# Optimization experiments

Measured on AMD Instinct MI355X. Metric: run time of the kernel, lower is better.

Reference implementation:

```python
import jax, jax.numpy as jnp
import numpy as np

EPS = 1e-5

def group_norm(x, w, b, groups):
    B, C, H, W = x.shape
    xg = x.reshape(B, groups, -1)
    mu = xg.mean(-1, keepdims=True)
    var = xg.var(-1, keepdims=True)
    xn = ((xg - mu) * jax.lax.rsqrt(var + EPS)).reshape(B, C, H, W)
    return xn * w[None, :, None, None] + b[None, :, None, None]

def gelu(x):
    return jax.nn.gelu(x, approximate=False)

def setup_inputs() -> dict:
    key = jax.random.key(0)
    ks = iter(jax.random.split(key, 64))
    B, H, W = 16, 64, 64
    dims = [128, 256, 512]
    hid = [32, 64, 128]  # max(d//4,16)
    total = 896
    sq = 112  # 896 // 8
    inp = {}
    inp["d0"] = jax.random.normal(next(ks), (B, dims[0], H, W), jnp.float32)
    inp["d1"] = jax.random.normal(next(ks), (B, dims[1], H, W), jnp.float32)
    inp["d2"] = jax.random.normal(next(ks), (B, dims[2], H, W), jnp.float32)
    for i, d in enumerate(dims):
        inp[f"gn{i}_w"] = jnp.ones((d,), jnp.float32)
        inp[f"gn{i}_b"] = jnp.zeros((d,), jnp.float32)
        inp[f"g{i}_w1"] = jax.random.normal(next(ks), (hid[i], d), jnp.float32) * 0.02
        inp[f"g{i}_b1"] = jnp.zeros((hid[i],), jnp.float32)
        inp[f"g{i}_w2"] = jax.random.normal(next(ks), (d, hid[i]), jnp.float32) * 0.02
        inp[f"g{i}_b2"] = jnp.zeros((d,), jnp.float32)
    inp["cn_w"] = jnp.ones((total,), jnp.float32)
    inp["cn_b"] = jnp.zeros((total,), jnp.float32)
    for name in ("ge", "le"):
        inp[f"{name}_w1"] = jax.random.normal(next(ks), (sq, total), jnp.float32) * 0.02
        inp[f"{name}_b1"] = jnp.zeros((sq,), jnp.float32)
        inp[f"{name}_w2"] = jax.random.normal(next(ks), (total, sq), jnp.float32) * 0.02
        inp[f"{name}_b2"] = jnp.zeros((total,), jnp.float32)
    inp["r_w"] = jax.random.normal(next(ks), (2, total), jnp.float32) * 0.02
    inp["r_b"] = jnp.zeros((2,), jnp.float32)
    inp["temp"] = jnp.ones((1,), jnp.float32)
    inp["gamma"] = jnp.ones((1,), jnp.float32) * 0.1
    return inp

def reference(d0, d1, d2,
              gn0_w, gn0_b, gn1_w, gn1_b, gn2_w, gn2_b,
              g0_w1, g0_b1, g0_w2, g0_b2,
              g1_w1, g1_b1, g1_w2, g1_b2,
              g2_w1, g2_b1, g2_w2, g2_b2,
              cn_w, cn_b,
              ge_w1, ge_b1, ge_w2, ge_b2,
              le_w1, le_b1, le_w2, le_b2,
              r_w, r_b, temp, gamma):
    def gate(d, w1, b1, w2, b2):
        p = d.mean((2, 3))                       # (B, C) avg pool
        g = jax.nn.sigmoid(gelu(p @ w1.T + b1) @ w2.T + b2)
        return d * g[:, :, None, None]

    d0 = group_norm(d0, gn0_w, gn0_b, 32)
    d1 = group_norm(d1, gn1_w, gn1_b, 32)
    d2 = group_norm(d2, gn2_w, gn2_b, 32)
    x = jnp.concatenate([
        gate(d0, g0_w1, g0_b1, g0_w2, g0_b2),
        gate(d1, g1_w1, g1_b1, g1_w2, g1_b2),
        gate(d2, g2_w1, g2_b1, g2_w2, g2_b2),
    ], axis=1)                                   # (B, 896, H, W)
    x = group_norm(x, cn_w, cn_b, 32)

    t = jnp.clip(temp, 0.5, 2.0)
    gp = x.mean((2, 3))                          # (B, 896) GAP
    mp = x.max((2, 3))                           # (B, 896) GMP
    w_global = jax.nn.sigmoid((gelu(gp @ ge_w1.T + ge_b1) @ ge_w2.T + ge_b2) / t)
    w_local = jax.nn.sigmoid((gelu(mp @ le_w1.T + le_b1) @ le_w2.T + le_b2) / t)
    route = jax.nn.softmax(gp @ r_w.T + r_b, axis=-1)   # (B, 2)
    alpha, beta = route[:, 0:1], route[:, 1:2]
    w_ch = alpha * w_global + beta * w_local * w_global
    return x * w_ch[:, :, None, None] + gamma * x
```

## Files before the change

### kernel.cpp

```cpp
#include <hip/hip_runtime.h>
#include <math.h>

#define HW   4096
#define NCH  896
#define NB   16

typedef float f4 __attribute__((ext_vector_type(4)));

__device__ __forceinline__ float gelu_exact(float x) {
    return 0.5f * x * (1.0f + erff(x * 0.70710678118654752440f));
}
__device__ __forceinline__ float sigmoidf_(float x) {
    return 1.0f / (1.0f + expf(-x));
}

__global__ __launch_bounds__(256) void stats_kernel(
    const float* __restrict__ d0, const float* __restrict__ d1,
    const float* __restrict__ d2,
    float* __restrict__ S, float* __restrict__ S2,
    float* __restrict__ MX, float* __restrict__ MN)
{
    const int wid  = (blockIdx.x << 2) + (threadIdx.x >> 6);
    const int lane = threadIdx.x & 63;
    const int b = wid / NCH;
    const int C = wid - b * NCH;
    const float* src; int cl, dim;
    if (C < 128)      { src = d0; cl = C;       dim = 128; }
    else if (C < 384) { src = d1; cl = C - 128; dim = 256; }
    else              { src = d2; cl = C - 384; dim = 512; }
    const f4* p = (const f4*)(src + ((size_t)b * dim + cl) * HW);

    float s = 0.f, s2 = 0.f, mx = -INFINITY, mn = INFINITY;
    #pragma unroll
    for (int k = 0; k < 16; ++k) {
        f4 v = p[lane + (k << 6)];
        s  += v.x + v.y + v.z + v.w;
        s2 += v.x*v.x + v.y*v.y + v.z*v.z + v.w*v.w;
        mx = fmaxf(mx, fmaxf(fmaxf(v.x, v.y), fmaxf(v.z, v.w)));
        mn = fminf(mn, fminf(fminf(v.x, v.y), fminf(v.z, v.w)));
    }
    #pragma unroll
    for (int off = 32; off > 0; off >>= 1) {
        s  += __shfl_xor(s,  off);
        s2 += __shfl_xor(s2, off);
        mx  = fmaxf(mx, __shfl_xor(mx, off));
        mn  = fminf(mn, __shfl_xor(mn, off));
    }
    if (lane == 0) {
        S [wid] = s;
        S2[wid] = s2;
        MX[wid] = mx;
        MN[wid] = mn;
    }
}

__global__ __launch_bounds__(256) void coeff_kernel(
    const float* __restrict__ S, const float* __restrict__ S2,
    const float* __restrict__ MX, const float* __restrict__ MN,
    const float* __restrict__ gn0w, const float* __restrict__ gn0b,
    const float* __restrict__ gn1w, const float* __restrict__ gn1b,
    const float* __restrict__ gn2w, const float* __restrict__ gn2b,
    const float* __restrict__ g0w1, const float* __restrict__ g0b1,
    const float* __restrict__ g0w2, const float* __restrict__ g0b2,
    const float* __restrict__ g1w1, const float* __restrict__ g1b1,
    const float* __restrict__ g1w2, const float* __restrict__ g1b2,
    const float* __restrict__ g2w1, const float* __restrict__ g2b1,
    const float* __restrict__ g2w2, const float* __restrict__ g2b2,
    const float* __restrict__ cnw,  const float* __restrict__ cnb,
    const float* __restrict__ gew1, const float* __restrict__ geb1,
    const float* __restrict__ gew2, const float* __restrict__ geb2,
    const float* __restrict__ lew1, const float* __restrict__ leb1,
    const float* __restrict__ lew2, const float* __restrict__ leb2,
    const float* __restrict__ rw,   const float* __restrict__ rb,
    const float* __restrict__ temp, const float* __restrict__ gamma,
    float* __restrict__ AF, float* __restrict__ BF)
{
    const int b = blockIdx.x;
    const int t = threadIdx.x;

    __shared__ float sS[NCH], sS2[NCH], sMX[NCH], sMN[NCH];
    __shared__ float sP[NCH], sG[NCH], sA[NCH], sB[NCH];
    __shared__ float sGP[NCH], sMP[NCH];
    __shared__ float sMu[96], sRs[96], sMu2[32], sRs2[32];
    __shared__ float sH[224];
    __shared__ float sLog[2];

    for (int c = t; c < NCH; c += 256) {
        sS [c] = S [b*NCH + c];
        sS2[c] = S2[b*NCH + c];
        sMX[c] = MX[b*NCH + c];
        sMN[c] = MN[b*NCH + c];
    }
    __syncthreads();

    if (t < 96) {
        const int i = t >> 5, g = t & 31;
        const int cpg = (i == 0) ? 4 : (i == 1) ? 8 : 16;
        const int off = (i == 0) ? 0 : (i == 1) ? 128 : 384;
        const int base = off + g * cpg;
        float ss = 0.f, ss2 = 0.f;
        for (int k = 0; k < cpg; ++k) { ss += sS[base + k]; ss2 += sS2[base + k]; }
        const float invN = 1.0f / (cpg * (float)HW);
        const float mu = ss * invN;
        const float var = ss2 * invN - mu * mu;
        sMu[t] = mu;
        sRs[t] = rsqrtf(var + 1e-5f);
    }
    __syncthreads();

    for (int c = t; c < NCH; c += 256) {
        int i, cl, cpg; const float *gw, *gb;
        if (c < 128)      { i = 0; cl = c;       cpg = 4;  gw = gn0w; gb = gn0b; }
        else if (c < 384) { i = 1; cl = c - 128; cpg = 8;  gw = gn1w; gb = gn1b; }
        else              { i = 2; cl = c - 384; cpg = 16; gw = gn2w; gb = gn2b; }
        const int gi = (i << 5) + cl / cpg;
        sP[c] = (sS[c] * (1.0f / HW) - sMu[gi]) * sRs[gi] * gw[cl] + gb[cl];
    }
    __syncthreads();

    if (t < 224) {
        int h, d, off; const float *w1, *b1;
        if (t < 32)      { h = t;      d = 128; off = 0;   w1 = g0w1; b1 = g0b1; }
        else if (t < 96) { h = t - 32; d = 256; off = 128; w1 = g1w1; b1 = g1b1; }
        else             { h = t - 96; d = 512; off = 384; w1 = g2w1; b1 = g2b1; }
        float acc = b1[h];
        const float* wr = w1 + (size_t)h * d;
        for (int c = 0; c < d; ++c) acc += sP[off + c] * wr[c];
        sH[t] = gelu_exact(acc);
    }
    __syncthreads();

    for (int c = t; c < NCH; c += 256) {
        int cl, hid, hoff; const float *w2, *b2;
        if (c < 128)      { cl = c;       hid = 32;  hoff = 0;  w2 = g0w2; b2 = g0b2; }
        else if (c < 384) { cl = c - 128; hid = 64;  hoff = 32; w2 = g1w2; b2 = g1b2; }
        else              { cl = c - 384; hid = 128; hoff = 96; w2 = g2w2; b2 = g2b2; }
        float acc = b2[cl];
        const float* wr = w2 + (size_t)cl * hid;
        for (int u = 0; u < hid; ++u) acc += sH[hoff + u] * wr[u];
        sG[c] = sigmoidf_(acc);
    }
    __syncthreads();

    for (int c = t; c < NCH; c += 256) {
        int i, cl, cpg; const float *gw, *gb;
        if (c < 128)      { i = 0; cl = c;       cpg = 4;  gw = gn0w; gb = gn0b; }
        else if (c < 384) { i = 1; cl = c - 128; cpg = 8;  gw = gn1w; gb = gn1b; }
        else              { i = 2; cl = c - 384; cpg = 16; gw = gn2w; gb = gn2b; }
        const int gi = (i << 5) + cl / cpg;
        const float mu = sMu[gi], rs = sRs[gi];
        const float a0 = rs * gw[cl];
        const float gch = sG[c];
        const float A = a0 * gch;
        const float B = (gb[cl] - mu * a0) * gch;
        sA[c] = A; sB[c] = B;
        const float s1 = sS[c], s2v = sS2[c];
        sP[c] = A * s1 + B * (float)HW;
        sG[c] = A * A * s2v + 2.0f * A * B * s1 + B * B * (float)HW;
    }
    __syncthreads();

    if (t < 32) {
        float ss = 0.f, ss2 = 0.f;
        const int base = t * 28;
        for (int k = 0; k < 28; ++k) { ss += sP[base + k]; ss2 += sG[base + k]; }
        const float invN = 1.0f / (28.0f * (float)HW);
        const float mu = ss * invN;
        const float var = ss2 * invN - mu * mu;
        sMu2[t] = mu;
        sRs2[t] = rsqrtf(var + 1e-5f);
    }
    __syncthreads();

    for (int c = t; c < NCH; c += 256) {
        const int g2 = c / 28;
        const float mu2 = sMu2[g2], rs2 = sRs2[g2];
        const float w = cnw[c] * rs2;
        const float a2 = sA[c] * w;
        const float b2v = (sB[c] - mu2) * w + cnb[c];
        sA[c] = a2; sB[c] = b2v;
        sGP[c] = a2 * (sS[c] * (1.0f / HW)) + b2v;
        sMP[c] = (a2 >= 0.f) ? (a2 * sMX[c] + b2v) : (a2 * sMN[c] + b2v);
    }
    __syncthreads();

    if (t < 224) {
        int q; const float *w1, *b1, *src;
        if (t < 112) { q = t;       w1 = gew1; b1 = geb1; src = sGP; }
        else         { q = t - 112; w1 = lew1; b1 = leb1; src = sMP; }
        float acc = b1[q];
        const float* wr = w1 + (size_t)q * NCH;
        for (int c = 0; c < NCH; ++c) acc += src[c] * wr[c];
        sH[t] = gelu_exact(acc);
    }
    if (t == 224 || t == 225) {
        const int r = t - 224;
        float acc = rb[r];
        const float* wr = rw + r * NCH;
        for (int c = 0; c < NCH; ++c) acc += sGP[c] * wr[c];
        sLog[r] = acc;
    }
    __syncthreads();

    const float tclip = fminf(fmaxf(temp[0], 0.5f), 2.0f);
    const float invt = 1.0f / tclip;
    const float l0 = sLog[0], l1 = sLog[1];
    const float m = fmaxf(l0, l1);
    const float e0 = expf(l0 - m), e1 = expf(l1 - m);
    const float alpha = e0 / (e0 + e1), beta = e1 / (e0 + e1);
    const float gam = gamma[0];
    for (int c = t; c < NCH; c += 256) {
        float accg = geb2[c], accl = leb2[c];
        const float* wgr = gew2 + (size_t)c * 112;
        const float* wlr = lew2 + (size_t)c * 112;
        for (int u = 0; u < 112; ++u) {
            accg += sH[u]       * wgr[u];
            accl += sH[112 + u] * wlr[u];
        }
        const float wgv = sigmoidf_(accg * invt);
        const float wlv = sigmoidf_(accl * invt);
        const float wch = alpha * wgv + beta * wlv * wgv;
        const float sc = wch + gam;
        AF[b*NCH + c] = sA[c] * sc;
        BF[b*NCH + c] = sB[c] * sc;
    }
}

__global__ __launch_bounds__(256) void apply_kernel(
    const float* __restrict__ d0, const float* __restrict__ d1,
    const float* __restrict__ d2,
    const float* __restrict__ AF, const float* __restrict__ BF,
    float* __restrict__ out)
{
    const int wid  = (blockIdx.x << 2) + (threadIdx.x >> 6);
    const int lane = threadIdx.x & 63;
    const int b = wid / NCH;
    const int C = wid - b * NCH;
    const float* src; int cl, dim;
    if (C < 128)      { src = d0; cl = C;       dim = 128; }
    else if (C < 384) { src = d1; cl = C - 128; dim = 256; }
    else              { src = d2; cl = C - 384; dim = 512; }
    const f4* pin = (const f4*)(src + ((size_t)b * dim + cl) * HW);
    f4* pout = (f4*)(out + (size_t)wid * HW);
    const float a  = AF[wid];
    const float bb = BF[wid];
    #pragma unroll
    for (int k = 0; k < 16; ++k) {
        f4 v = __builtin_nontemporal_load(&pin[lane + (k << 6)]);
        v = v * a + bb;
        __builtin_nontemporal_store(v, &pout[lane + (k << 6)]);
    }
}

extern "C" void kernel_launch(void* const* d_in, const int* in_sizes, int n_in,
                              void* d_out, int out_size, void* d_ws, size_t ws_size,
                              hipStream_t stream) {
    const float* d0   = (const float*)d_in[0];
    const float* d1   = (const float*)d_in[1];
    const float* d2   = (const float*)d_in[2];
    const float* gn0w = (const float*)d_in[3];
    const float* gn0b = (const float*)d_in[4];
    const float* g0w1 = (const float*)d_in[5];
    const float* g0b1 = (const float*)d_in[6];
    const float* g0w2 = (const float*)d_in[7];
    const float* g0b2 = (const float*)d_in[8];
    const float* gn1w = (const float*)d_in[9];
    const float* gn1b = (const float*)d_in[10];
    const float* g1w1 = (const float*)d_in[11];
    const float* g1b1 = (const float*)d_in[12];
    const float* g1w2 = (const float*)d_in[13];
    const float* g1b2 = (const float*)d_in[14];
    const float* gn2w = (const float*)d_in[15];
    const float* gn2b = (const float*)d_in[16];
    const float* g2w1 = (const float*)d_in[17];
    const float* g2b1 = (const float*)d_in[18];
    const float* g2w2 = (const float*)d_in[19];
    const float* g2b2 = (const float*)d_in[20];
    const float* cnw  = (const float*)d_in[21];
    const float* cnb  = (const float*)d_in[22];
    const float* gew1 = (const float*)d_in[23];
    const float* geb1 = (const float*)d_in[24];
    const float* gew2 = (const float*)d_in[25];
    const float* geb2 = (const float*)d_in[26];
    const float* lew1 = (const float*)d_in[27];
    const float* leb1 = (const float*)d_in[28];
    const float* lew2 = (const float*)d_in[29];
    const float* leb2 = (const float*)d_in[30];
    const float* rw   = (const float*)d_in[31];
    const float* rb   = (const float*)d_in[32];
    const float* temp = (const float*)d_in[33];
    const float* gamma= (const float*)d_in[34];

    float* S  = (float*)d_ws;
    float* S2 = S  + NB * NCH;
    float* MX = S2 + NB * NCH;
    float* MN = MX + NB * NCH;
    float* AF = MN + NB * NCH;
    float* BF = AF + NB * NCH;

    stats_kernel<<<(NB * NCH) / 4, 256, 0, stream>>>(d0, d1, d2, S, S2, MX, MN);
    coeff_kernel<<<NB, 256, 0, stream>>>(
        S, S2, MX, MN,
        gn0w, gn0b, gn1w, gn1b, gn2w, gn2b,
        g0w1, g0b1, g0w2, g0b2,
        g1w1, g1b1, g1w2, g1b2,
        g2w1, g2b1, g2w2, g2b2,
        cnw, cnb,
        gew1, geb1, gew2, geb2,
        lew1, leb1, lew2, leb2,
        rw, rb, temp, gamma, AF, BF);
    apply_kernel<<<(NB * NCH) / 4, 256, 0, stream>>>(d0, d1, d2, AF, BF, (float*)d_out);
}
```

Baseline: 592.2 us.

## Split serial coefficient kernel into three multi-block kernels for MLP parallelism

The single 16-block coefficient kernel is split into three stages: per-batch norm folding, a 112-block kernel computing the squeeze MLP hidden layer with 8 lanes per hidden unit, and a 112-block kernel for the expand layer and final scale. Previously each batch's 896x224 dot products ran on one block with one thread per output, which left most of the GPU idle on a latency-bound section. In exchange there are two extra launches and intermediates round-trip through the workspace, which reuses the stats buffers in place (restrict removed on those pointers).

```diff
diff --git a/kernel.cpp b/kernel.cpp
--- a/kernel.cpp
+++ b/kernel.cpp
@@ -54,9 +54,9 @@
     }
 }
 
-__global__ __launch_bounds__(256) void coeff_kernel(
-    const float* __restrict__ S, const float* __restrict__ S2,
-    const float* __restrict__ MX, const float* __restrict__ MN,
+__global__ __launch_bounds__(256) void coeffA_kernel(
+    const float* S, const float* S2,
+    const float* MX, const float* MN,
     const float* __restrict__ gn0w, const float* __restrict__ gn0b,
     const float* __restrict__ gn1w, const float* __restrict__ gn1b,
     const float* __restrict__ gn2w, const float* __restrict__ gn2b,
@@ -67,20 +67,16 @@
     const float* __restrict__ g2w1, const float* __restrict__ g2b1,
     const float* __restrict__ g2w2, const float* __restrict__ g2b2,
     const float* __restrict__ cnw,  const float* __restrict__ cnb,
-    const float* __restrict__ gew1, const float* __restrict__ geb1,
-    const float* __restrict__ gew2, const float* __restrict__ geb2,
-    const float* __restrict__ lew1, const float* __restrict__ leb1,
-    const float* __restrict__ lew2, const float* __restrict__ leb2,
     const float* __restrict__ rw,   const float* __restrict__ rb,
-    const float* __restrict__ temp, const float* __restrict__ gamma,
-    float* __restrict__ AF, float* __restrict__ BF)
+    float* wA, float* wB, float* wGP, float* wMP,
+    float* __restrict__ wAB)
 {
     const int b = blockIdx.x;
     const int t = threadIdx.x;
 
     __shared__ float sS[NCH], sS2[NCH], sMX[NCH], sMN[NCH];
     __shared__ float sP[NCH], sG[NCH], sA[NCH], sB[NCH];
-    __shared__ float sGP[NCH], sMP[NCH];
+    __shared__ float sGP[NCH];
     __shared__ float sMu[96], sRs[96], sMu2[32], sRs2[32];
     __shared__ float sH[224];
     __shared__ float sLog[2];
@@ -178,51 +174,103 @@
         const float w = cnw[c] * rs2;
         const float a2 = sA[c] * w;
         const float b2v = (sB[c] - mu2) * w + cnb[c];
-        sA[c] = a2; sB[c] = b2v;
-        sGP[c] = a2 * (sS[c] * (1.0f / HW)) + b2v;
-        sMP[c] = (a2 >= 0.f) ? (a2 * sMX[c] + b2v) : (a2 * sMN[c] + b2v);
-    }
-    __syncthreads();
-
-    if (t < 224) {
-        int q; const float *w1, *b1, *src;
-        if (t < 112) { q = t;       w1 = gew1; b1 = geb1; src = sGP; }
-        else         { q = t - 112; w1 = lew1; b1 = leb1; src = sMP; }
-        float acc = b1[q];
-        const float* wr = w1 + (size_t)q * NCH;
-        for (int c = 0; c < NCH; ++c) acc += src[c] * wr[c];
-        sH[t] = gelu_exact(acc);
-    }
-    if (t == 224 || t == 225) {
-        const int r = t - 224;
-        float acc = rb[r];
-        const float* wr = rw + r * NCH;
+        const float gp = a2 * (sS[c] * (1.0f / HW)) + b2v;
+        const float mp = (a2 >= 0.f) ? (a2 * sMX[c] + b2v) : (a2 * sMN[c] + b2v);
+        sGP[c] = gp;
+        wA [b*NCH + c] = a2;
+        wB [b*NCH + c] = b2v;
+        wGP[b*NCH + c] = gp;
+        wMP[b*NCH + c] = mp;
+    }
+    __syncthreads();
+
+    if (t == 0 || t == 1) {
+        float acc = rb[t];
+        const float* wr = rw + t * NCH;
         for (int c = 0; c < NCH; ++c) acc += sGP[c] * wr[c];
-        sLog[r] = acc;
-    }
-    __syncthreads();
-
-    const float tclip = fminf(fmaxf(temp[0], 0.5f), 2.0f);
-    const float invt = 1.0f / tclip;
-    const float l0 = sLog[0], l1 = sLog[1];
-    const float m = fmaxf(l0, l1);
-    const float e0 = expf(l0 - m), e1 = expf(l1 - m);
-    const float alpha = e0 / (e0 + e1), beta = e1 / (e0 + e1);
-    const float gam = gamma[0];
-    for (int c = t; c < NCH; c += 256) {
+        sLog[t] = acc;
+    }
+    __syncthreads();
+    if (t == 0) {
+        const float l0 = sLog[0], l1 = sLog[1];
+        const float m = fmaxf(l0, l1);
+        const float e0 = expf(l0 - m), e1 = expf(l1 - m);
+        wAB[b*2 + 0] = e0 / (e0 + e1);
+        wAB[b*2 + 1] = e1 / (e0 + e1);
+    }
+}
+
+__global__ __launch_bounds__(256) void coeffB1_kernel(
+    const float* __restrict__ wGP, const float* __restrict__ wMP,
+    const float* __restrict__ gew1, const float* __restrict__ geb1,
+    const float* __restrict__ lew1, const float* __restrict__ leb1,
+    float* __restrict__ wH)
+{
+    const int b = blockIdx.x / 7;
+    const int j = blockIdx.x - b * 7;
+    const int t = threadIdx.x;
+    __shared__ float sGPl[NCH], sMPl[NCH];
+    for (int c = t; c < NCH; c += 256) {
+        sGPl[c] = wGP[b*NCH + c];
+        sMPl[c] = wMP[b*NCH + c];
+    }
+    __syncthreads();
+
+    const int g = t >> 3;
+    const int i = t & 7;
+    const int unit = j * 32 + g;
+    const float* srcv; const float* w1; const float* b1; int q;
+    if (unit < 112) { q = unit;       srcv = sGPl; w1 = gew1; b1 = geb1; }
+    else            { q = unit - 112; srcv = sMPl; w1 = lew1; b1 = leb1; }
+    const float* wr = w1 + (size_t)q * NCH;
+
+    float acc = 0.f;
+    #pragma unroll 4
+    for (int cc = 0; cc < 112; ++cc) {
+        const int c = (cc << 3) + i;
+        acc += srcv[c] * wr[c];
+    }
+    acc += __shfl_down(acc, 4, 8);
+    acc += __shfl_down(acc, 2, 8);
+    acc += __shfl_down(acc, 1, 8);
+    if (i == 0) wH[b*224 + unit] = gelu_exact(acc + b1[q]);
+}
+
+__global__ __launch_bounds__(256) void coeffB2_kernel(
+    const float* __restrict__ wA,  const float* __restrict__ wB,
+    const float* __restrict__ wH,  const float* __restrict__ wAB,
+    const float* __restrict__ gew2, const float* __restrict__ geb2,
+    const float* __restrict__ lew2, const float* __restrict__ leb2,
+    const float* __restrict__ temp, const float* __restrict__ gamma,
+    float* __restrict__ AF, float* __restrict__ BF)
+{
+    const int b = blockIdx.x / 7;
+    const int j = blockIdx.x - b * 7;
+    const int t = threadIdx.x;
+    __shared__ float sHl[224];
+    if (t < 224) sHl[t] = wH[b*224 + t];
+    __syncthreads();
+
+    if (t < 128) {
+        const int c = j * 128 + t;
+        const float tclip = fminf(fmaxf(temp[0], 0.5f), 2.0f);
+        const float invt = 1.0f / tclip;
+        const float alpha = wAB[b*2 + 0];
+        const float beta  = wAB[b*2 + 1];
         float accg = geb2[c], accl = leb2[c];
         const float* wgr = gew2 + (size_t)c * 112;
         const float* wlr = lew2 + (size_t)c * 112;
+        #pragma unroll 4
         for (int u = 0; u < 112; ++u) {
-            accg += sH[u]       * wgr[u];
-            accl += sH[112 + u] * wlr[u];
+            accg += sHl[u]       * wgr[u];
+            accl += sHl[112 + u] * wlr[u];
         }
         const float wgv = sigmoidf_(accg * invt);
         const float wlv = sigmoidf_(accl * invt);
         const float wch = alpha * wgv + beta * wlv * wgv;
-        const float sc = wch + gam;
-        AF[b*NCH + c] = sA[c] * sc;
-        BF[b*NCH + c] = sB[c] * sc;
+        const float sc = wch + gamma[0];
+        AF[b*NCH + c] = wA[b*NCH + c] * sc;
+        BF[b*NCH + c] = wB[b*NCH + c] * sc;
     }
 }
 
@@ -291,23 +339,28 @@
     const float* temp = (const float*)d_in[33];
     const float* gamma= (const float*)d_in[34];
 
+    const int N = NB * NCH;
     float* S  = (float*)d_ws;
-    float* S2 = S  + NB * NCH;
-    float* MX = S2 + NB * NCH;
-    float* MN = MX + NB * NCH;
-    float* AF = MN + NB * NCH;
-    float* BF = AF + NB * NCH;
+    float* S2 = S  + N;
+    float* MX = S2 + N;
+    float* MN = MX + N;
+    float* AF = MN + N;
+    float* BF = AF + N;
+    float* wH  = BF + N;
+    float* wAB = wH + NB * 224;
 
     stats_kernel<<<(NB * NCH) / 4, 256, 0, stream>>>(d0, d1, d2, S, S2, MX, MN);
-    coeff_kernel<<<NB, 256, 0, stream>>>(
+    coeffA_kernel<<<NB, 256, 0, stream>>>(
         S, S2, MX, MN,
         gn0w, gn0b, gn1w, gn1b, gn2w, gn2b,
         g0w1, g0b1, g0w2, g0b2,
         g1w1, g1b1, g1w2, g1b2,
         g2w1, g2b1, g2w2, g2b2,
-        cnw, cnb,
-        gew1, geb1, gew2, geb2,
-        lew1, leb1, lew2, leb2,
-        rw, rb, temp, gamma, AF, BF);
+        cnw, cnb, rw, rb,
+        S, S2, MX, MN, wAB);
+    coeffB1_kernel<<<NB * 7, 256, 0, stream>>>(
+        MX, MN, gew1, geb1, lew1, leb1, wH);
+    coeffB2_kernel<<<NB * 7, 256, 0, stream>>>(
+        S, S2, wH, wAB, gew2, geb2, lew2, leb2, temp, gamma, AF, BF);
     apply_kernel<<<(NB * NCH) / 4, 256, 0, stream>>>(d0, d1, d2, AF, BF, (float*)d_out);
 }
```

Result: faster. 553.0 us (-6.6%).
